# Kernel optimization log

Hardware: AMD Instinct MI355X
Metric: run time of the kernel (lower is better)

Reference implementation:

```python
import jax, jax.numpy as jnp
import numpy as np

H = 64  # hidden_size


def _lstm_layer(x, Wih, Whh, bih, bhh):
    """One LSTM layer, batch_first. x: [B,T,I] -> h_seq: [B,T,H].
    PyTorch gate order: i, f, g, o."""
    B = x.shape[0]
    # Precompute input contribution for all timesteps: [B,T,4H]
    xg = jnp.einsum('bti,gi->btg', x, Wih) + bih + bhh
    xg = jnp.swapaxes(xg, 0, 1)  # [T,B,4H] for scan

    def step(carry, xg_t):
        h, c = carry
        gates = xg_t + h @ Whh.T  # [B,4H]
        i, f, g, o = jnp.split(gates, 4, axis=-1)
        i = jax.nn.sigmoid(i)
        f = jax.nn.sigmoid(f)
        g = jnp.tanh(g)
        o = jax.nn.sigmoid(o)
        c = f * c + i * g
        h = o * jnp.tanh(c)
        return (h, c), h

    h0 = jnp.zeros((B, H), dtype=x.dtype)
    c0 = jnp.zeros((B, H), dtype=x.dtype)
    (_, _), h_seq = jax.lax.scan(step, (h0, c0), xg)
    return jnp.swapaxes(h_seq, 0, 1)  # [B,T,H]


def setup_inputs() -> dict:
    key = jax.random.key(0)
    ks = jax.random.split(key, 11)
    B, T, I, O = 2048, 512, 6, 6
    s = 1.0 / np.sqrt(H)
    u = lambda k, shape: jax.random.uniform(k, shape, jnp.float32, -s, s)
    return {
        'x': jax.random.normal(ks[0], (B, T, I), jnp.float32),
        'Wih0': u(ks[1], (4 * H, I)),
        'Whh0': u(ks[2], (4 * H, H)),
        'bih0': u(ks[3], (4 * H,)),
        'bhh0': u(ks[4], (4 * H,)),
        'Wih1': u(ks[5], (4 * H, H)),
        'Whh1': u(ks[6], (4 * H, H)),
        'bih1': u(ks[7], (4 * H,)),
        'bhh1': u(ks[8], (4 * H,)),
        'Wlin': u(ks[9], (O, H)),
        'blin': u(ks[10], (O,)),
    }


def reference(x, Wih0, Whh0, bih0, bhh0, Wih1, Whh1, bih1, bhh1, Wlin, blin):
    h1 = _lstm_layer(x, Wih0, Whh0, bih0, bhh0)   # [B,T,H]
    h2 = _lstm_layer(h1, Wih1, Whh1, bih1, bhh1)  # [B,T,H]
    return h2[:, -1, :] @ Wlin.T + blin           # [B,O]
```

## Files before the change

### kernel.cpp

```cpp
#include <hip/hip_runtime.h>

typedef _Float16 f16;
typedef _Float16 f16x2 __attribute__((ext_vector_type(2)));
typedef _Float16 f16x4 __attribute__((ext_vector_type(4)));
typedef _Float16 f16x8 __attribute__((ext_vector_type(8)));
typedef float f32x4 __attribute__((ext_vector_type(4)));
typedef unsigned int u32x4 __attribute__((ext_vector_type(4)));

#define NLOG2E -1.4426950408889634f
#define NC2LE  -2.8853900817779268f

__device__ __forceinline__ float fastrcp(float x) { return __builtin_amdgcn_rcpf(x); }
__device__ __forceinline__ float fexp2(float x) { return __builtin_amdgcn_exp2f(x); }

#define TT 512
#define NB 8
#define XBS 3080
#define XS_ELE (NB * XBS)
#define AUGS 184
#define A0OFF XS_ELE
#define A1OFF (A0OFF + NB * AUGS)
#define LDS_F16 (A1OFF + NB * AUGS)
#define LDS_BYTES (LDS_F16 * 2)

__device__ __forceinline__ f16x8 cvt8s(const float* p, float s) {
  f32x4 a = *(const f32x4*)p;
  f32x4 b = *(const f32x4*)(p + 4);
  f16x8 r;
  #pragma unroll
  for (int i = 0; i < 4; ++i) { r[i] = (f16)(a[i] * s); r[4 + i] = (f16)(b[i] * s); }
  return r;
}

__global__ __launch_bounds__(512, 2)
void lstm2_kernel(const float* __restrict__ x,
                  const float* __restrict__ Wih0, const float* __restrict__ Whh0,
                  const float* __restrict__ bih0, const float* __restrict__ bhh0,
                  const float* __restrict__ Wih1, const float* __restrict__ Whh1,
                  const float* __restrict__ bih1, const float* __restrict__ bhh1,
                  const float* __restrict__ Wlin, const float* __restrict__ blin,
                  float* __restrict__ out)
{
  extern __shared__ f16 lds[];
  f16* xstage = lds;
  f16* aug0 = lds + A0OFF;
  f16* aug1 = lds + A1OFF;
  const unsigned int* xw = (const unsigned int*)xstage;

  const int tid = threadIdx.x;
  const int wv = tid >> 6;
  const int team = wv >> 2;
  const int uw = wv & 3;
  const int lane = tid & 63;
  const int m = lane & 15;
  const int q = lane >> 4;
  const bool lohalf = (m < 8);
  const int bcol = m & 7;

  f16x8 af[4][4];
  f32x4 bv[4];
  #pragma unroll
  for (int g = 0; g < 4; ++g) {
    const float sg = (g == 2) ? NC2LE : NLOG2E;
    const int R = g * 64 + 16 * uw + m;
    if (team == 1) {
      af[g][0] = cvt8s(&Whh1[R * 64 + 8 * q], sg);
      af[g][1] = cvt8s(&Whh1[R * 64 + 32 + 8 * q], sg);
      af[g][2] = cvt8s(&Wih1[R * 64 + 8 * q], sg);
      af[g][3] = cvt8s(&Wih1[R * 64 + 32 + 8 * q], sg);
    } else {
      af[g][0] = cvt8s(&Whh0[R * 64 + 8 * q], sg);
      af[g][1] = cvt8s(&Whh0[R * 64 + 32 + 8 * q], sg);
      f16x8 t;
      #pragma unroll
      for (int i = 0; i < 8; ++i) t[i] = (f16)0.0f;
      if (q == 0) {
        #pragma unroll
        for (int i = 0; i < 6; ++i) t[i] = (f16)(Wih0[R * 6 + i] * sg);
      }
      af[g][2] = t;
    }
    const float* bi = (team == 1) ? bih1 : bih0;
    const float* bh = (team == 1) ? bhh1 : bhh0;
    const int U = g * 64 + 16 * uw + 4 * q;
    #pragma unroll
    for (int r = 0; r < 4; ++r) bv[g][r] = (bi[U + r] + bh[U + r]) * sg;
  }

  {
    const float* xblk = x + (size_t)blockIdx.x * (NB * TT * 6);
    #pragma unroll 1
    for (int n = 0; n < NB; ++n) {
      const float* src = xblk + n * (TT * 6);
      f16* dst = xstage + n * XBS;
      for (int idx = tid; idx < TT * 6 / 4; idx += 512) {
        f32x4 v = *(const f32x4*)&src[idx * 4];
        f16x4 h;
        #pragma unroll
        for (int i = 0; i < 4; ++i) h[i] = (f16)v[i];
        *(f16x4*)&dst[idx * 4] = h;
      }
    }
  }
  for (int idx = tid; idx < NB * AUGS; idx += 512) aug0[idx] = (f16)0.0f;
  __syncthreads();

  float cs0 = 0.0f, cs1 = 0.0f;

  const int colb = bcol * AUGS;
  const int xdw = bcol * (XBS / 2);
  const int rowofs = 16 * uw + 4 * q + (lohalf ? 0 : 2);

  auto fin_pre = [&](float ai, float afv, float ag, float ao, float& cs,
                     float& so_o, float& cn_o) {
    float A = 1.0f + fexp2(ai);
    float B = 1.0f + fexp2(afv);
    float G = 1.0f + fexp2(ag);
    float O = 1.0f + fexp2(ao);
    float d1 = fastrcp(A * B);
    float d2 = fastrcp(G * O);
    float si = d1 * B;
    float sf = d1 * A;
    float tg = __builtin_fmaf(2.0f, d2 * O, -1.0f);
    float so = d2 * G;
    float cn = __builtin_fmaf(sf, cs, si * tg);
    cs = cn;
    so_o = so; cn_o = cn;
  };

  auto compact_finish = [&](const f32x4* acc) -> f16x2 {
    float u0[4], u1[4];
    #pragma unroll
    for (int g = 0; g < 4; ++g) {
      u0[g] = lohalf ? acc[g][0] : acc[g][2];
      u1[g] = lohalf ? acc[g][1] : acc[g][3];
    }
    float so0, cn0, so1, cn1;
    fin_pre(u0[0], u0[1], u0[2], u0[3], cs0, so0, cn0);
    fin_pre(u1[0], u1[1], u1[2], u1[3], cs1, so1, cn1);
    float T0 = 1.0f + fexp2(cn0 * NC2LE);
    float T1 = 1.0f + fexp2(cn1 * NC2LE);
    float h0 = __builtin_fmaf(2.0f * so0, fastrcp(T0), -so0);
    float h1 = __builtin_fmaf(2.0f * so1, fastrcp(T1), -so1);
    return __builtin_bit_cast(f16x2, __builtin_amdgcn_cvt_pkrtz(h0, h1));
  };

  auto STEP = [&](f16* cur, f16* nxt, int t) {
    if (team == 1) {
      f16x8 Bh1a = *(const f16x8*)&cur[colb + 64 + 8 * q];
      f16x8 Bh1b = *(const f16x8*)&cur[colb + 96 + 8 * q];
      f16x8 Bh2a = *(const f16x8*)&cur[colb + 0 + 8 * q];
      f16x8 Bh2b = *(const f16x8*)&cur[colb + 32 + 8 * q];
      f32x4 acc[4];
      #pragma unroll
      for (int g = 0; g < 4; ++g) {
        f32x4 p = __builtin_amdgcn_mfma_f32_16x16x32_f16(af[g][0], Bh2a, bv[g], 0, 0, 0);
        p = __builtin_amdgcn_mfma_f32_16x16x32_f16(af[g][1], Bh2b, p, 0, 0, 0);
        p = __builtin_amdgcn_mfma_f32_16x16x32_f16(af[g][2], Bh1a, p, 0, 0, 0);
        acc[g] = __builtin_amdgcn_mfma_f32_16x16x32_f16(af[g][3], Bh1b, p, 0, 0, 0);
      }
      f16x2 h2o = compact_finish(acc);
      *(f16x2*)&nxt[colb + rowofs] = h2o;
    } else {
      const int xo = xdw + 3 * (t + 1);
      u32x4 uv;
      uv[0] = xw[xo]; uv[1] = xw[xo + 1]; uv[2] = xw[xo + 2]; uv[3] = 0u;
      f16x8 Bh1a = *(const f16x8*)&cur[colb + 64 + 8 * q];
      f16x8 Bh1b = *(const f16x8*)&cur[colb + 96 + 8 * q];
      f16x8 bx = __builtin_bit_cast(f16x8, uv);
      f32x4 acc[4];
      #pragma unroll
      for (int g = 0; g < 4; ++g) {
        f32x4 p = __builtin_amdgcn_mfma_f32_16x16x32_f16(af[g][0], Bh1a, bv[g], 0, 0, 0);
        p = __builtin_amdgcn_mfma_f32_16x16x32_f16(af[g][1], Bh1b, p, 0, 0, 0);
        acc[g] = __builtin_amdgcn_mfma_f32_16x16x32_f16(af[g][2], bx, p, 0, 0, 0);
      }
      f16x2 h1o = compact_finish(acc);
      *(f16x2*)&nxt[colb + 64 + rowofs] = h1o;
    }
    __syncthreads();
  };

  if (team == 0) {
    u32x4 uv;
    uv[0] = xw[xdw + 0]; uv[1] = xw[xdw + 1]; uv[2] = xw[xdw + 2]; uv[3] = 0u;
    f16x8 bx = __builtin_bit_cast(f16x8, uv);
    f32x4 acc[4];
    #pragma unroll
    for (int g = 0; g < 4; ++g)
      acc[g] = __builtin_amdgcn_mfma_f32_16x16x32_f16(af[g][2], bx, bv[g], 0, 0, 0);
    f16x2 h1o = compact_finish(acc);
    *(f16x2*)&aug0[colb + 64 + rowofs] = h1o;
  }
  __syncthreads();

  #pragma unroll 1
  for (int t = 0; t < TT - 2; t += 2) {
    STEP(aug0, aug1, t);
    STEP(aug1, aug0, t + 1);
  }
  STEP(aug0, aug1, TT - 2);

  if (team == 1) {
    f16x8 Bh2a = *(const f16x8*)&aug1[colb + 0 + 8 * q];
    f16x8 Bh2b = *(const f16x8*)&aug1[colb + 32 + 8 * q];
    f16x8 Bh1a = *(const f16x8*)&aug1[colb + 64 + 8 * q];
    f16x8 Bh1b = *(const f16x8*)&aug1[colb + 96 + 8 * q];
    f32x4 acc[4];
    #pragma unroll
    for (int g = 0; g < 4; ++g) {
      f32x4 p = __builtin_amdgcn_mfma_f32_16x16x32_f16(af[g][0], Bh2a, bv[g], 0, 0, 0);
      p = __builtin_amdgcn_mfma_f32_16x16x32_f16(af[g][1], Bh2b, p, 0, 0, 0);
      p = __builtin_amdgcn_mfma_f32_16x16x32_f16(af[g][2], Bh1a, p, 0, 0, 0);
      acc[g] = __builtin_amdgcn_mfma_f32_16x16x32_f16(af[g][3], Bh1b, p, 0, 0, 0);
    }
    f16x2 h2o = compact_finish(acc);
    *(f16x2*)&aug0[colb + rowofs] = h2o;
  }
  __syncthreads();

  if (tid < 48) {
    const int bl = tid / 6, o = tid - bl * 6;
    float s = blin[o];
    const float* wl = &Wlin[o * 64];
    #pragma unroll 8
    for (int u = 0; u < 64; ++u) s += wl[u] * (float)aug0[bl * AUGS + u];
    out[(blockIdx.x * NB + bl) * 6 + o] = s;
  }
}

extern "C" void kernel_launch(void* const* d_in, const int* in_sizes, int n_in,
                              void* d_out, int out_size, void* d_ws, size_t ws_size,
                              hipStream_t stream) {
  const float* xp    = (const float*)d_in[0];
  const float* Wih0  = (const float*)d_in[1];
  const float* Whh0  = (const float*)d_in[2];
  const float* bih0  = (const float*)d_in[3];
  const float* bhh0  = (const float*)d_in[4];
  const float* Wih1  = (const float*)d_in[5];
  const float* Whh1  = (const float*)d_in[6];
  const float* bih1  = (const float*)d_in[7];
  const float* bhh1  = (const float*)d_in[8];
  const float* Wlin  = (const float*)d_in[9];
  const float* blin  = (const float*)d_in[10];
  float* outp = (float*)d_out;

  hipFuncSetAttribute(reinterpret_cast<const void*>(lstm2_kernel),
                      hipFuncAttributeMaxDynamicSharedMemorySize, LDS_BYTES);
  lstm2_kernel<<<256, 512, LDS_BYTES, stream>>>(xp, Wih0, Whh0, bih0, bhh0,
                                                Wih1, Whh1, bih1, bhh1,
                                                Wlin, blin, outp);
}
```

Baseline: 275.4 us.

## Replace per-step block barriers with LDS ring buffer and flag-based producer/consumer sync

Replaces the lockstep __syncthreads after every timestep with a 4-deep LDS ring of hidden states and per-wave progress flags, so the layer-0 team can run ahead of the layer-1 team by up to the ring depth. Each wave spins on volatile LDS flags with s_sleep before consuming, and signals after writing. This aims to remove full-block barrier stalls and let the two layers' work overlap. The risks are spin-loop overhead, memory-ordering subtleties on LDS, and the bounded spin iteration cap.

```diff
diff --git a/kernel.cpp b/kernel.cpp
--- a/kernel.cpp
+++ b/kernel.cpp
@@ -18,9 +18,11 @@
 #define XBS 3080
 #define XS_ELE (NB * XBS)
 #define AUGS 184
-#define A0OFF XS_ELE
-#define A1OFF (A0OFF + NB * AUGS)
-#define LDS_F16 (A1OFF + NB * AUGS)
+#define R 4
+#define RINGS (NB * AUGS)
+#define RING_OFF XS_ELE
+#define FLAG_OFF (RING_OFF + R * RINGS)
+#define LDS_F16 (FLAG_OFF + 16)
 #define LDS_BYTES (LDS_F16 * 2)
 
 __device__ __forceinline__ f16x8 cvt8s(const float* p, float s) {
@@ -43,8 +45,9 @@
 {
   extern __shared__ f16 lds[];
   f16* xstage = lds;
-  f16* aug0 = lds + A0OFF;
-  f16* aug1 = lds + A1OFF;
+  f16* ring = lds + RING_OFF;
+  volatile unsigned* p0 = (volatile unsigned*)(lds + FLAG_OFF);
+  volatile unsigned* p1 = p0 + 4;
   const unsigned int* xw = (const unsigned int*)xstage;
 
   const int tid = threadIdx.x;
@@ -62,23 +65,24 @@
   #pragma unroll
   for (int g = 0; g < 4; ++g) {
     const float sg = (g == 2) ? NC2LE : NLOG2E;
-    const int R = g * 64 + 16 * uw + m;
+    const int Rw = g * 64 + 16 * uw + m;
     if (team == 1) {
-      af[g][0] = cvt8s(&Whh1[R * 64 + 8 * q], sg);
-      af[g][1] = cvt8s(&Whh1[R * 64 + 32 + 8 * q], sg);
-      af[g][2] = cvt8s(&Wih1[R * 64 + 8 * q], sg);
-      af[g][3] = cvt8s(&Wih1[R * 64 + 32 + 8 * q], sg);
+      af[g][0] = cvt8s(&Whh1[Rw * 64 + 8 * q], sg);
+      af[g][1] = cvt8s(&Whh1[Rw * 64 + 32 + 8 * q], sg);
+      af[g][2] = cvt8s(&Wih1[Rw * 64 + 8 * q], sg);
+      af[g][3] = cvt8s(&Wih1[Rw * 64 + 32 + 8 * q], sg);
     } else {
-      af[g][0] = cvt8s(&Whh0[R * 64 + 8 * q], sg);
-      af[g][1] = cvt8s(&Whh0[R * 64 + 32 + 8 * q], sg);
+      af[g][0] = cvt8s(&Whh0[Rw * 64 + 8 * q], sg);
+      af[g][1] = cvt8s(&Whh0[Rw * 64 + 32 + 8 * q], sg);
       f16x8 t;
       #pragma unroll
       for (int i = 0; i < 8; ++i) t[i] = (f16)0.0f;
       if (q == 0) {
         #pragma unroll
-        for (int i = 0; i < 6; ++i) t[i] = (f16)(Wih0[R * 6 + i] * sg);
+        for (int i = 0; i < 6; ++i) t[i] = (f16)(Wih0[Rw * 6 + i] * sg);
       }
       af[g][2] = t;
+      af[g][3] = t;
     }
     const float* bi = (team == 1) ? bih1 : bih0;
     const float* bh = (team == 1) ? bhh1 : bhh0;
@@ -102,11 +106,11 @@
       }
     }
   }
-  for (int idx = tid; idx < NB * AUGS; idx += 512) aug0[idx] = (f16)0.0f;
+  for (int idx = tid; idx < R * RINGS; idx += 512) ring[idx] = (f16)0.0f;
+  if (tid < 8) ((volatile unsigned*)(lds + FLAG_OFF))[tid] = 0u;
   __syncthreads();
 
   float cs0 = 0.0f, cs1 = 0.0f;
-
   const int colb = bcol * AUGS;
   const int xdw = bcol * (XBS / 2);
   const int rowofs = 16 * uw + 4 * q + (lohalf ? 0 : 2);
@@ -145,23 +149,41 @@
     return __builtin_bit_cast(f16x2, __builtin_amdgcn_cvt_pkrtz(h0, h1));
   };
 
-  auto STEP = [&](f16* cur, f16* nxt, int t) {
-    if (team == 1) {
-      f16x8 Bh1a = *(const f16x8*)&cur[colb + 64 + 8 * q];
-      f16x8 Bh1b = *(const f16x8*)&cur[colb + 96 + 8 * q];
-      f16x8 Bh2a = *(const f16x8*)&cur[colb + 0 + 8 * q];
-      f16x8 Bh2b = *(const f16x8*)&cur[colb + 32 + 8 * q];
+  auto spin2 = [&](int t0, int t1) {
+    for (int it = 0; it < (1 << 20); ++it) {
+      unsigned a0 = p0[0], a1 = p0[1], a2 = p0[2], a3 = p0[3];
+      unsigned b0 = p1[0], b1 = p1[1], b2 = p1[2], b3 = p1[3];
+      int m0 = (int)min(min(a0, a1), min(a2, a3));
+      int m1 = (int)min(min(b0, b1), min(b2, b3));
+      if (m0 >= t0 && m1 >= t1) break;
+      __builtin_amdgcn_s_sleep(1);
+    }
+    asm volatile("" ::: "memory");
+  };
+
+  auto signal = [&](volatile unsigned* p, unsigned val) {
+    asm volatile("s_waitcnt lgkmcnt(0)" ::: "memory");
+    if (lane == 0) p[uw] = val;
+  };
+
+  if (team == 0) {
+    {
+      u32x4 uv;
+      uv[0] = xw[xdw + 0]; uv[1] = xw[xdw + 1]; uv[2] = xw[xdw + 2]; uv[3] = 0u;
+      f16x8 bx = __builtin_bit_cast(f16x8, uv);
       f32x4 acc[4];
       #pragma unroll
-      for (int g = 0; g < 4; ++g) {
-        f32x4 p = __builtin_amdgcn_mfma_f32_16x16x32_f16(af[g][0], Bh2a, bv[g], 0, 0, 0);
-        p = __builtin_amdgcn_mfma_f32_16x16x32_f16(af[g][1], Bh2b, p, 0, 0, 0);
-        p = __builtin_amdgcn_mfma_f32_16x16x32_f16(af[g][2], Bh1a, p, 0, 0, 0);
-        acc[g] = __builtin_amdgcn_mfma_f32_16x16x32_f16(af[g][3], Bh1b, p, 0, 0, 0);
-      }
-      f16x2 h2o = compact_finish(acc);
-      *(f16x2*)&nxt[colb + rowofs] = h2o;
-    } else {
+      for (int g = 0; g < 4; ++g)
+        acc[g] = __builtin_amdgcn_mfma_f32_16x16x32_f16(af[g][2], bx, bv[g], 0, 0, 0);
+      f16x2 h1o = compact_finish(acc);
+      *(f16x2*)&ring[0 * RINGS + colb + 64 + rowofs] = h1o;
+      signal(p0, 1u);
+    }
+    #pragma unroll 1
+    for (int t = 0; t < TT - 1; ++t) {
+      spin2(t + 1, t + 2 - R);
+      f16* cur = ring + (t & (R - 1)) * RINGS;
+      f16* nxt = ring + ((t + 1) & (R - 1)) * RINGS;
       const int xo = xdw + 3 * (t + 1);
       u32x4 uv;
       uv[0] = xw[xo]; uv[1] = xw[xo + 1]; uv[2] = xw[xo + 2]; uv[3] = 0u;
@@ -177,54 +199,40 @@
       }
       f16x2 h1o = compact_finish(acc);
       *(f16x2*)&nxt[colb + 64 + rowofs] = h1o;
-    }
-    __syncthreads();
-  };
-
-  if (team == 0) {
-    u32x4 uv;
-    uv[0] = xw[xdw + 0]; uv[1] = xw[xdw + 1]; uv[2] = xw[xdw + 2]; uv[3] = 0u;
-    f16x8 bx = __builtin_bit_cast(f16x8, uv);
-    f32x4 acc[4];
-    #pragma unroll
-    for (int g = 0; g < 4; ++g)
-      acc[g] = __builtin_amdgcn_mfma_f32_16x16x32_f16(af[g][2], bx, bv[g], 0, 0, 0);
-    f16x2 h1o = compact_finish(acc);
-    *(f16x2*)&aug0[colb + 64 + rowofs] = h1o;
+      signal(p0, (unsigned)(t + 2));
+    }
+  } else {
+    #pragma unroll 1
+    for (int t = 0; t < TT; ++t) {
+      spin2(t + 1, t);
+      f16* sh1 = ring + (t & (R - 1)) * RINGS;
+      f16* sh2 = ring + ((t - 1 + R) & (R - 1)) * RINGS;
+      f16x8 Bh2a = *(const f16x8*)&sh2[colb + 0 + 8 * q];
+      f16x8 Bh2b = *(const f16x8*)&sh2[colb + 32 + 8 * q];
+      f16x8 Bh1a = *(const f16x8*)&sh1[colb + 64 + 8 * q];
+      f16x8 Bh1b = *(const f16x8*)&sh1[colb + 96 + 8 * q];
+      f32x4 acc[4];
+      #pragma unroll
+      for (int g = 0; g < 4; ++g) {
+        f32x4 p = __builtin_amdgcn_mfma_f32_16x16x32_f16(af[g][0], Bh2a, bv[g], 0, 0, 0);
+        p = __builtin_amdgcn_mfma_f32_16x16x32_f16(af[g][1], Bh2b, p, 0, 0, 0);
+        p = __builtin_amdgcn_mfma_f32_16x16x32_f16(af[g][2], Bh1a, p, 0, 0, 0);
+        acc[g] = __builtin_amdgcn_mfma_f32_16x16x32_f16(af[g][3], Bh1b, p, 0, 0, 0);
+      }
+      f16x2 h2o = compact_finish(acc);
+      *(f16x2*)&sh1[colb + 0 + rowofs] = h2o;
+      signal(p1, (unsigned)(t + 1));
+    }
   }
   __syncthreads();
 
-  #pragma unroll 1
-  for (int t = 0; t < TT - 2; t += 2) {
-    STEP(aug0, aug1, t);
-    STEP(aug1, aug0, t + 1);
-  }
-  STEP(aug0, aug1, TT - 2);
-
-  if (team == 1) {
-    f16x8 Bh2a = *(const f16x8*)&aug1[colb + 0 + 8 * q];
-    f16x8 Bh2b = *(const f16x8*)&aug1[colb + 32 + 8 * q];
-    f16x8 Bh1a = *(const f16x8*)&aug1[colb + 64 + 8 * q];
-    f16x8 Bh1b = *(const f16x8*)&aug1[colb + 96 + 8 * q];
-    f32x4 acc[4];
-    #pragma unroll
-    for (int g = 0; g < 4; ++g) {
-      f32x4 p = __builtin_amdgcn_mfma_f32_16x16x32_f16(af[g][0], Bh2a, bv[g], 0, 0, 0);
-      p = __builtin_amdgcn_mfma_f32_16x16x32_f16(af[g][1], Bh2b, p, 0, 0, 0);
-      p = __builtin_amdgcn_mfma_f32_16x16x32_f16(af[g][2], Bh1a, p, 0, 0, 0);
-      acc[g] = __builtin_amdgcn_mfma_f32_16x16x32_f16(af[g][3], Bh1b, p, 0, 0, 0);
-    }
-    f16x2 h2o = compact_finish(acc);
-    *(f16x2*)&aug0[colb + rowofs] = h2o;
-  }
-  __syncthreads();
-
   if (tid < 48) {
+    const f16* hfin = ring + ((TT - 1) & (R - 1)) * RINGS;
     const int bl = tid / 6, o = tid - bl * 6;
     float s = blin[o];
     const float* wl = &Wlin[o * 64];
     #pragma unroll 8
-    for (int u = 0; u < 64; ++u) s += wl[u] * (float)aug0[bl * AUGS + u];
+    for (int u = 0; u < 64; ++u) s += wl[u] * (float)hfin[bl * AUGS + u];
     out[(blockIdx.x * NB + bl) * 6 + o] = s;
   }
 }
```

Measured after the change: 458.3 us. 66.4% more time.
